# Kernel optimization log

Hardware: AMD Instinct MI355X
Metric: run time of the kernel (lower is better)

The kernel has to match this reference:

```python
import jax, jax.numpy as jnp
import numpy as np
from jax import lax

B, T, D, R, V = 128, 8, 2048, 4, 512

def setup_inputs() -> dict:
    key = jax.random.key(0)
    k0, k1, k2, k3, k4 = jax.random.split(key, 5)
    # scales chosen so the TT products stay within fp32 range (see notes)
    input_embs = jax.random.normal(k0, (B, T, D), dtype=jnp.float32) * 0.1
    label_ids = jax.random.randint(k1, (B, T), 0, V)
    w_alpha = jax.random.normal(k2, (D, R), dtype=jnp.float32) * 0.04
    w_beta = jax.random.normal(k3, (D, R), dtype=jnp.float32) * 0.04
    w_vocab = jax.random.normal(k4, (D, V * R * R), dtype=jnp.float32) * 0.04
    return {"input_embs": input_embs, "label_ids": label_ids,
            "w_alpha": w_alpha, "w_beta": w_beta, "w_vocab": w_vocab}

def _tt_loss(input_embs, w_alpha, w_beta, w_vocab, label_ids):
    b, t, d = input_embs.shape
    flat = input_embs.reshape(-1, d)                    # [B*T, D]
    alpha = jnp.abs((flat @ w_alpha).reshape(b, t, R).mean(1))   # [B, R]
    beta = jnp.abs((flat @ w_beta).reshape(b, t, R).mean(1))     # [B, R]
    core = jnp.abs((flat @ w_vocab).reshape(b, t, R, V, R).mean(1))  # [B, R, V, R]

    # --- _select: gather per-position R x R cores and chain-multiply ---
    core_v = core.transpose(0, 2, 1, 3)                 # [B, V, R, R]
    sel = jnp.take_along_axis(core_v, label_ids[:, :, None, None], axis=1)  # [B, T, R, R]
    sel_t = jnp.swapaxes(sel, 0, 1)                     # [T, B, R, R]

    def chain(carry, m):
        return jnp.einsum('bik,bkj->bij', carry, m), None
    res, _ = lax.scan(chain, sel_t[0], sel_t[1:])       # [B, R, R]
    u = jnp.einsum('bi,bij,bj->b', alpha, res, beta)    # unnormalized probs [B]

    # --- normalization constant: marg^(T+1) contracted with alpha/beta ---
    marg = core.sum(2)                                  # [B, R, R]

    def pow_step(c, _):
        return jnp.einsum('bik,bkj->bij', c, marg), None
    zmat, _ = lax.scan(pow_step, marg, None, length=t)  # marg^(t+1)
    z = jnp.einsum('bi,bij,bj->b', alpha, zmat, beta)

    loss = -jnp.log(u / z)
    return loss.mean()

def reference(input_embs, label_ids, w_alpha, w_beta, w_vocab):
    return _tt_loss(input_embs, w_alpha, w_beta, w_vocab, label_ids)
```

## Files before the change

kernel.cpp:

```cpp
#include <hip/hip_runtime.h>
#include <math.h>

#define BB 128
#define TT 8
#define DD 2048
#define RR 4
#define VV 512

typedef __attribute__((ext_vector_type(8))) short short8;
typedef __attribute__((ext_vector_type(4))) float v4f;

__device__ __forceinline__ unsigned pack_bf16(float x, float y) {
    union { float f; unsigned u; } a, b;
    a.f = x; b.f = y;
    unsigned ua = a.u + 0x7fffu + ((a.u >> 16) & 1u);
    unsigned ub = b.u + 0x7fffu + ((b.u >> 16) & 1u);
    return (ua >> 16) | (ub & 0xffff0000u);
}

__global__ __launch_bounds__(256) void phaseA(const float* __restrict__ inp,
                                              const float* __restrict__ w_alpha,
                                              const float* __restrict__ w_beta,
                                              unsigned short* __restrict__ fmb,
                                              float* __restrict__ alphaP,
                                              float* __restrict__ betaP,
                                              float* __restrict__ marg) {
    int bid = blockIdx.x;
    int b = bid >> 1, half = bid & 1;
    int tid = threadIdx.x;

    if (bid < 8) marg[bid * 256 + tid] = 0.f;

    const float* base = inp + (size_t)b * TT * DD;
    float pa[4] = {0.f, 0.f, 0.f, 0.f};
    float pb[4] = {0.f, 0.f, 0.f, 0.f};
#pragma unroll
    for (int i = 0; i < 4; ++i) {
        int d = half * 1024 + i * 256 + tid;
        float s = 0.f;
#pragma unroll
        for (int t = 0; t < TT; ++t) s += base[t * DD + d];
        float v = s * (1.0f / TT);
        union { float f; unsigned u; } cv; cv.f = v;
        unsigned r = cv.u + 0x7fffu + ((cv.u >> 16) & 1u);
        fmb[b * DD + d] = (unsigned short)(r >> 16);
        float4 wa = *(const float4*)(w_alpha + d * 4);
        float4 wb = *(const float4*)(w_beta + d * 4);
        pa[0] += v * wa.x; pa[1] += v * wa.y; pa[2] += v * wa.z; pa[3] += v * wa.w;
        pb[0] += v * wb.x; pb[1] += v * wb.y; pb[2] += v * wb.z; pb[3] += v * wb.w;
    }
#pragma unroll
    for (int r = 0; r < 4; ++r) {
        for (int m = 1; m < 64; m <<= 1) {
            pa[r] += __shfl_xor(pa[r], m);
            pb[r] += __shfl_xor(pb[r], m);
        }
    }
    __shared__ float sA[4][4], sB[4][4];
    int wid = tid >> 6;
    if ((tid & 63) == 0) {
#pragma unroll
        for (int r = 0; r < 4; ++r) { sA[wid][r] = pa[r]; sB[wid][r] = pb[r]; }
    }
    __syncthreads();
    if (tid < 4) {
        alphaP[b * 8 + half * 4 + tid] = sA[0][tid] + sA[1][tid] + sA[2][tid] + sA[3][tid];
        betaP [b * 8 + half * 4 + tid] = sB[0][tid] + sB[1][tid] + sB[2][tid] + sB[3][tid];
    }
}

__global__ __launch_bounds__(512, 2) void phaseB(const unsigned short* __restrict__ fmb,
                                                 const float* __restrict__ wv,
                                                 const int* __restrict__ labels,
                                                 float* __restrict__ margA,
                                                 float* __restrict__ sel) {
    __shared__ unsigned short Ws[2][32][136];
    __shared__ int slab[BB * TT];

    const int tid = threadIdx.x;
    const int nb = blockIdx.x;
    const int col0 = nb * 32;

    slab[tid] = labels[tid];
    slab[tid + 512] = labels[tid + 512];

    const int nq = tid & 7;
    const int kp = tid >> 3;
    const int w = tid >> 6;
    const int lane = tid & 63;
    const int m15 = lane & 15;
    const int q = lane >> 4;

    const float* wbase = wv + (size_t)(2 * kp) * 8192 + col0 + nq * 4;
    const unsigned short* abase = fmb + (w * 16 + m15) * DD + q * 8;

    v4f acc0 = {0.f, 0.f, 0.f, 0.f};
    v4f acc1 = {0.f, 0.f, 0.f, 0.f};
    short8 afrA[4], afrB[4];
    float4 swA0, swA1, swB0, swB1;

    swA0 = *(const float4*)(wbase);
    swA1 = *(const float4*)(wbase + 8192);
    {
        const float* p = wbase + (size_t)128 * 8192;
        swB0 = *(const float4*)(p);
        swB1 = *(const float4*)(p + 8192);
    }
#pragma unroll
    for (int ks = 0; ks < 4; ++ks) afrA[ks] = *(const short8*)(abase + ks * 32);
    {
        const float* f0 = (const float*)&swA0;
        const float* f1 = (const float*)&swA1;
#pragma unroll
        for (int j = 0; j < 4; ++j)
            *(unsigned*)&Ws[0][nq * 4 + j][2 * kp] = pack_bf16(f0[j], f1[j]);
    }
    __syncthreads();

    for (int i = 0; i < 8; ++i) {
        const int c0 = 2 * i;
        if (c0 < 14) {
            const float* p = wbase + (size_t)(c0 + 2) * 128 * 8192;
            swA0 = *(const float4*)(p);
            swA1 = *(const float4*)(p + 8192);
        }
        {
            const unsigned short* ap = abase + (c0 + 1) * 128;
#pragma unroll
            for (int ks = 0; ks < 4; ++ks) afrB[ks] = *(const short8*)(ap + ks * 32);
        }
#pragma unroll
        for (int ks = 0; ks < 4; ++ks) {
            short8 b0 = *(const short8*)&Ws[0][m15][ks * 32 + q * 8];
            short8 b1 = *(const short8*)&Ws[0][16 + m15][ks * 32 + q * 8];
            acc0 = __builtin_amdgcn_mfma_f32_16x16x32_bf16(afrA[ks], b0, acc0, 0, 0, 0);
            acc1 = __builtin_amdgcn_mfma_f32_16x16x32_bf16(afrA[ks], b1, acc1, 0, 0, 0);
        }
        {
            const float* f0 = (const float*)&swB0;
            const float* f1 = (const float*)&swB1;
#pragma unroll
            for (int j = 0; j < 4; ++j)
                *(unsigned*)&Ws[1][nq * 4 + j][2 * kp] = pack_bf16(f0[j], f1[j]);
        }
        __syncthreads();

        const int c1 = 2 * i + 1;
        if (c1 < 14) {
            const float* p = wbase + (size_t)(c1 + 2) * 128 * 8192;
            swB0 = *(const float4*)(p);
            swB1 = *(const float4*)(p + 8192);
        }
        if (c1 < 15) {
            const unsigned short* ap = abase + (c1 + 1) * 128;
#pragma unroll
            for (int ks = 0; ks < 4; ++ks) afrA[ks] = *(const short8*)(ap + ks * 32);
        }
#pragma unroll
        for (int ks = 0; ks < 4; ++ks) {
            short8 b0 = *(const short8*)&Ws[1][m15][ks * 32 + q * 8];
            short8 b1 = *(const short8*)&Ws[1][16 + m15][ks * 32 + q * 8];
            acc0 = __builtin_amdgcn_mfma_f32_16x16x32_bf16(afrB[ks], b0, acc0, 0, 0, 0);
            acc1 = __builtin_amdgcn_mfma_f32_16x16x32_bf16(afrB[ks], b1, acc1, 0, 0, 0);
        }
        if (c1 < 15) {
            const float* f0 = (const float*)&swA0;
            const float* f1 = (const float*)&swA1;
#pragma unroll
            for (int j = 0; j < 4; ++j)
                *(unsigned*)&Ws[0][nq * 4 + j][2 * kp] = pack_bf16(f0[j], f1[j]);
        }
        __syncthreads();
    }

    const int vbase = (nb & 63) * 8;
    const int iblk = nb >> 6;
    const int j = m15 & 3;
    const int v0 = vbase + (m15 >> 2);
    const float* a0p = (const float*)&acc0;
    const float* a1p = (const float*)&acc1;
#pragma unroll
    for (int r = 0; r < 4; ++r) {
        int m = w * 16 + q * 4 + r;
        float a0 = fabsf(a0p[r]);
        float a1 = fabsf(a1p[r]);
        float s = a0 + a1;
        s += __shfl_xor(s, 4);
        s += __shfl_xor(s, 8);
        if ((lane & 12) == 0) atomicAdd(&margA[m * 16 + iblk * 4 + j], s);
#pragma unroll
        for (int t = 0; t < TT; ++t) {
            int lv = slab[m * 8 + t];
            if (lv == v0)     sel[(m * 8 + t) * 16 + iblk * 4 + j] = a0;
            if (lv == v0 + 4) sel[(m * 8 + t) * 16 + iblk * 4 + j] = a1;
        }
    }
}

__global__ __launch_bounds__(128) void phaseD(const float* __restrict__ alphaP,
                                              const float* __restrict__ betaP,
                                              const float* __restrict__ marg,
                                              const float* __restrict__ sel,
                                              float* __restrict__ out) {
    int b = threadIdx.x;
    const float* sb = sel + b * TT * 16;
    float res[16], tmp[16], mm[16], zm[16];
#pragma unroll
    for (int e = 0; e < 16; ++e) res[e] = sb[e];
    for (int t = 1; t < TT; ++t) {
        const float* m = sb + t * 16;
#pragma unroll
        for (int i = 0; i < 4; ++i)
#pragma unroll
            for (int jj = 0; jj < 4; ++jj) {
                float s = 0.f;
#pragma unroll
                for (int k = 0; k < 4; ++k) s += res[i * 4 + k] * m[k * 4 + jj];
                tmp[i * 4 + jj] = s;
            }
#pragma unroll
        for (int e = 0; e < 16; ++e) res[e] = tmp[e];
    }
#pragma unroll
    for (int e = 0; e < 16; ++e) { mm[e] = marg[b * 16 + e]; zm[e] = mm[e]; }
    for (int st = 0; st < TT; ++st) {
#pragma unroll
        for (int i = 0; i < 4; ++i)
#pragma unroll
            for (int jj = 0; jj < 4; ++jj) {
                float s = 0.f;
#pragma unroll
                for (int k = 0; k < 4; ++k) s += zm[i * 4 + k] * mm[k * 4 + jj];
                tmp[i * 4 + jj] = s;
            }
#pragma unroll
        for (int e = 0; e < 16; ++e) zm[e] = tmp[e];
    }
    float u = 0.f, z = 0.f;
#pragma unroll
    for (int i = 0; i < 4; ++i) {
        float ai = fabsf(alphaP[b * 8 + i] + alphaP[b * 8 + 4 + i]);
#pragma unroll
        for (int jj = 0; jj < 4; ++jj) {
            float bj = fabsf(betaP[b * 8 + jj] + betaP[b * 8 + 4 + jj]);
            u += ai * res[i * 4 + jj] * bj;
            z += ai * zm[i * 4 + jj] * bj;
        }
    }
    float loss = logf(z) - logf(u);
    __shared__ float red[128];
    red[b] = loss;
    __syncthreads();
    for (int off = 64; off >= 1; off >>= 1) {
        if (b < off) red[b] += red[b + off];
        __syncthreads();
    }
    if (b == 0) out[0] = red[0] * (1.0f / BB);
}

extern "C" void kernel_launch(void* const* d_in, const int* in_sizes, int n_in,
                              void* d_out, int out_size, void* d_ws, size_t ws_size,
                              hipStream_t stream) {
    const float* inp     = (const float*)d_in[0];
    const int*   labels  = (const int*)d_in[1];
    const float* w_alpha = (const float*)d_in[2];
    const float* w_beta  = (const float*)d_in[3];
    const float* wv      = (const float*)d_in[4];
    float* out = (float*)d_out;

    float* ws     = (float*)d_ws;
    float* alphaP = ws;
    float* betaP  = ws + 1024;
    float* marg   = ws + 2048;
    float* sel    = ws + 4096;
    unsigned short* fmb = (unsigned short*)(ws + 20480);

    phaseA<<<256, 256, 0, stream>>>(inp, w_alpha, w_beta, fmb, alphaP, betaP, marg);
    phaseB<<<256, 512, 0, stream>>>(fmb, wv, labels, marg, sel);
    phaseD<<<1, 128, 0, stream>>>(alphaP, betaP, marg, sel, out);
}
```

Before: 122.6 us.

## Narrow phaseB column tiles to 16 and double K-chunk per stage with 512 blocks

The vocab GEMM kernel now handles 16 output columns per block instead of 32 and stages 256-row K chunks instead of 128. This doubles the grid to 512 blocks, and blocks are remapped so that neighbouring block IDs take columns spread across the weight matrix. The goal is more parallelism across CUs and fewer pipeline stages and barriers. In exchange, each block loads the full bf16 activation matrix, so activation traffic doubles, and register pressure rises from the 8-wide A fragments.

Measured after the change: 140.9 us. 14.9% more time.

```diff
diff --git a/kernel.cpp b/kernel.cpp
--- a/kernel.cpp
+++ b/kernel.cpp
@@ -69,23 +69,24 @@
     }
 }
 
-__global__ __launch_bounds__(512, 2) void phaseB(const unsigned short* __restrict__ fmb,
+__global__ __launch_bounds__(512, 4) void phaseB(const unsigned short* __restrict__ fmb,
                                                  const float* __restrict__ wv,
                                                  const int* __restrict__ labels,
                                                  float* __restrict__ margA,
                                                  float* __restrict__ sel) {
-    __shared__ unsigned short Ws[2][32][136];
+    __shared__ unsigned short Ws[2][16][268];
     __shared__ int slab[BB * TT];
 
     const int tid = threadIdx.x;
-    const int nb = blockIdx.x;
-    const int col0 = nb * 32;
+    const int bid = blockIdx.x;
+    const int nb = ((bid & 7) << 6) | (bid >> 3);
+    const int col0 = nb * 16;
 
     slab[tid] = labels[tid];
     slab[tid + 512] = labels[tid + 512];
 
-    const int nq = tid & 7;
-    const int kp = tid >> 3;
+    const int nq = tid & 3;
+    const int kp = tid >> 2;
     const int w = tid >> 6;
     const int lane = tid & 63;
     const int m15 = lane & 15;
@@ -94,20 +95,19 @@
     const float* wbase = wv + (size_t)(2 * kp) * 8192 + col0 + nq * 4;
     const unsigned short* abase = fmb + (w * 16 + m15) * DD + q * 8;
 
-    v4f acc0 = {0.f, 0.f, 0.f, 0.f};
-    v4f acc1 = {0.f, 0.f, 0.f, 0.f};
-    short8 afrA[4], afrB[4];
+    v4f acc = {0.f, 0.f, 0.f, 0.f};
+    short8 afrA[8], afrB[8];
     float4 swA0, swA1, swB0, swB1;
 
     swA0 = *(const float4*)(wbase);
     swA1 = *(const float4*)(wbase + 8192);
     {
-        const float* p = wbase + (size_t)128 * 8192;
+        const float* p = wbase + (size_t)256 * 8192;
         swB0 = *(const float4*)(p);
         swB1 = *(const float4*)(p + 8192);
     }
 #pragma unroll
-    for (int ks = 0; ks < 4; ++ks) afrA[ks] = *(const short8*)(abase + ks * 32);
+    for (int ks = 0; ks < 8; ++ks) afrA[ks] = *(const short8*)(abase + ks * 32);
     {
         const float* f0 = (const float*)&swA0;
         const float* f1 = (const float*)&swA1;
@@ -117,24 +117,23 @@
     }
     __syncthreads();
 
-    for (int i = 0; i < 8; ++i) {
+#pragma unroll
+    for (int i = 0; i < 4; ++i) {
         const int c0 = 2 * i;
-        if (c0 < 14) {
-            const float* p = wbase + (size_t)(c0 + 2) * 128 * 8192;
+        if (c0 < 6) {
+            const float* p = wbase + (size_t)(c0 + 2) * 256 * 8192;
             swA0 = *(const float4*)(p);
             swA1 = *(const float4*)(p + 8192);
         }
         {
-            const unsigned short* ap = abase + (c0 + 1) * 128;
-#pragma unroll
-            for (int ks = 0; ks < 4; ++ks) afrB[ks] = *(const short8*)(ap + ks * 32);
-        }
-#pragma unroll
-        for (int ks = 0; ks < 4; ++ks) {
+            const unsigned short* ap = abase + (c0 + 1) * 256;
+#pragma unroll
+            for (int ks = 0; ks < 8; ++ks) afrB[ks] = *(const short8*)(ap + ks * 32);
+        }
+#pragma unroll
+        for (int ks = 0; ks < 8; ++ks) {
             short8 b0 = *(const short8*)&Ws[0][m15][ks * 32 + q * 8];
-            short8 b1 = *(const short8*)&Ws[0][16 + m15][ks * 32 + q * 8];
-            acc0 = __builtin_amdgcn_mfma_f32_16x16x32_bf16(afrA[ks], b0, acc0, 0, 0, 0);
-            acc1 = __builtin_amdgcn_mfma_f32_16x16x32_bf16(afrA[ks], b1, acc1, 0, 0, 0);
+            acc = __builtin_amdgcn_mfma_f32_16x16x32_bf16(afrA[ks], b0, acc, 0, 0, 0);
         }
         {
             const float* f0 = (const float*)&swB0;
@@ -146,24 +145,22 @@
         __syncthreads();
 
         const int c1 = 2 * i + 1;
-        if (c1 < 14) {
-            const float* p = wbase + (size_t)(c1 + 2) * 128 * 8192;
+        if (c1 < 6) {
+            const float* p = wbase + (size_t)(c1 + 2) * 256 * 8192;
             swB0 = *(const float4*)(p);
             swB1 = *(const float4*)(p + 8192);
         }
-        if (c1 < 15) {
-            const unsigned short* ap = abase + (c1 + 1) * 128;
-#pragma unroll
-            for (int ks = 0; ks < 4; ++ks) afrA[ks] = *(const short8*)(ap + ks * 32);
-        }
-#pragma unroll
-        for (int ks = 0; ks < 4; ++ks) {
-            short8 b0 = *(const short8*)&Ws[1][m15][ks * 32 + q * 8];
-            short8 b1 = *(const short8*)&Ws[1][16 + m15][ks * 32 + q * 8];
-            acc0 = __builtin_amdgcn_mfma_f32_16x16x32_bf16(afrB[ks], b0, acc0, 0, 0, 0);
-            acc1 = __builtin_amdgcn_mfma_f32_16x16x32_bf16(afrB[ks], b1, acc1, 0, 0, 0);
-        }
-        if (c1 < 15) {
+        if (c1 < 7) {
+            const unsigned short* ap = abase + (c1 + 1) * 256;
+#pragma unroll
+            for (int ks = 0; ks < 8; ++ks) afrA[ks] = *(const short8*)(ap + ks * 32);
+        }
+#pragma unroll
+        for (int ks = 0; ks < 8; ++ks) {
+            short8 b1 = *(const short8*)&Ws[1][m15][ks * 32 + q * 8];
+            acc = __builtin_amdgcn_mfma_f32_16x16x32_bf16(afrB[ks], b1, acc, 0, 0, 0);
+        }
+        if (c1 < 7) {
             const float* f0 = (const float*)&swA0;
             const float* f1 = (const float*)&swA1;
 #pragma unroll
@@ -173,26 +170,22 @@
         __syncthreads();
     }
 
-    const int vbase = (nb & 63) * 8;
-    const int iblk = nb >> 6;
+    const int i_out = nb >> 7;
     const int j = m15 & 3;
-    const int v0 = vbase + (m15 >> 2);
-    const float* a0p = (const float*)&acc0;
-    const float* a1p = (const float*)&acc1;
+    const int v0 = (nb & 127) * 4 + (m15 >> 2);
+    const float* ap = (const float*)&acc;
 #pragma unroll
     for (int r = 0; r < 4; ++r) {
         int m = w * 16 + q * 4 + r;
-        float a0 = fabsf(a0p[r]);
-        float a1 = fabsf(a1p[r]);
-        float s = a0 + a1;
+        float a0 = fabsf(ap[r]);
+        float s = a0;
         s += __shfl_xor(s, 4);
         s += __shfl_xor(s, 8);
-        if ((lane & 12) == 0) atomicAdd(&margA[m * 16 + iblk * 4 + j], s);
+        if ((lane & 12) == 0) atomicAdd(&margA[m * 16 + i_out * 4 + j], s);
 #pragma unroll
         for (int t = 0; t < TT; ++t) {
             int lv = slab[m * 8 + t];
-            if (lv == v0)     sel[(m * 8 + t) * 16 + iblk * 4 + j] = a0;
-            if (lv == v0 + 4) sel[(m * 8 + t) * 16 + iblk * 4 + j] = a1;
+            if (lv == v0) sel[(m * 8 + t) * 16 + i_out * 4 + j] = a0;
         }
     }
 }
@@ -276,6 +269,6 @@
     unsigned short* fmb = (unsigned short*)(ws + 20480);
 
     phaseA<<<256, 256, 0, stream>>>(inp, w_alpha, w_beta, fmb, alphaP, betaP, marg);
-    phaseB<<<256, 512, 0, stream>>>(fmb, wv, labels, marg, sel);
+    phaseB<<<512, 512, 0, stream>>>(fmb, wv, labels, marg, sel);
     phaseD<<<1, 128, 0, stream>>>(alphaP, betaP, marg, sel, out);
 }
```

## Split GEMM K dimension across two blocks and add reduction kernel for marg/sel

Applied to the files above, without the earlier changes.

The main GEMM kernel now splits the 2048-long reduction dimension into two halves, launching 512 blocks instead of 256 and raising the launch-bounds occupancy hint. Raw partial results are written to a workspace buffer. A new kernel sums the two partials, applies abs, computes the vocab-marginal and gathers the label-selected cores, replacing the atomics and label scan in the GEMM epilogue. This is meant to fill more compute units and shorten each block's serial K loop, at the cost of writing and rereading an 8 MB partial buffer and one extra launch.

Result: no change. 122.5 us (-0.1%).

```diff
diff --git a/kernel.cpp b/kernel.cpp
--- a/kernel.cpp
+++ b/kernel.cpp
@@ -23,13 +23,10 @@
                                               const float* __restrict__ w_beta,
                                               unsigned short* __restrict__ fmb,
                                               float* __restrict__ alphaP,
-                                              float* __restrict__ betaP,
-                                              float* __restrict__ marg) {
+                                              float* __restrict__ betaP) {
     int bid = blockIdx.x;
     int b = bid >> 1, half = bid & 1;
     int tid = threadIdx.x;
-
-    if (bid < 8) marg[bid * 256 + tid] = 0.f;
 
     const float* base = inp + (size_t)b * TT * DD;
     float pa[4] = {0.f, 0.f, 0.f, 0.f};
@@ -69,20 +66,16 @@
     }
 }
 
-__global__ __launch_bounds__(512, 2) void phaseB(const unsigned short* __restrict__ fmb,
+__global__ __launch_bounds__(512, 4) void phaseB(const unsigned short* __restrict__ fmb,
                                                  const float* __restrict__ wv,
-                                                 const int* __restrict__ labels,
-                                                 float* __restrict__ margA,
-                                                 float* __restrict__ sel) {
+                                                 float* __restrict__ Cpart) {
     __shared__ unsigned short Ws[2][32][136];
-    __shared__ int slab[BB * TT];
 
     const int tid = threadIdx.x;
-    const int nb = blockIdx.x;
-    const int col0 = nb * 32;
-
-    slab[tid] = labels[tid];
-    slab[tid + 512] = labels[tid + 512];
+    const int bid = blockIdx.x;
+    const int colb = bid & 255;
+    const int half = bid >> 8;
+    const int col0 = colb * 32;
 
     const int nq = tid & 7;
     const int kp = tid >> 3;
@@ -91,8 +84,8 @@
     const int m15 = lane & 15;
     const int q = lane >> 4;
 
-    const float* wbase = wv + (size_t)(2 * kp) * 8192 + col0 + nq * 4;
-    const unsigned short* abase = fmb + (w * 16 + m15) * DD + q * 8;
+    const float* wbase = wv + (size_t)(half * 1024 + 2 * kp) * 8192 + col0 + nq * 4;
+    const unsigned short* abase = fmb + (w * 16 + m15) * DD + half * 1024 + q * 8;
 
     v4f acc0 = {0.f, 0.f, 0.f, 0.f};
     v4f acc1 = {0.f, 0.f, 0.f, 0.f};
@@ -117,9 +110,10 @@
     }
     __syncthreads();
 
-    for (int i = 0; i < 8; ++i) {
+#pragma unroll
+    for (int i = 0; i < 4; ++i) {
         const int c0 = 2 * i;
-        if (c0 < 14) {
+        if (c0 < 6) {
             const float* p = wbase + (size_t)(c0 + 2) * 128 * 8192;
             swA0 = *(const float4*)(p);
             swA1 = *(const float4*)(p + 8192);
@@ -146,12 +140,12 @@
         __syncthreads();
 
         const int c1 = 2 * i + 1;
-        if (c1 < 14) {
+        if (c1 < 6) {
             const float* p = wbase + (size_t)(c1 + 2) * 128 * 8192;
             swB0 = *(const float4*)(p);
             swB1 = *(const float4*)(p + 8192);
         }
-        if (c1 < 15) {
+        if (c1 < 7) {
             const unsigned short* ap = abase + (c1 + 1) * 128;
 #pragma unroll
             for (int ks = 0; ks < 4; ++ks) afrA[ks] = *(const short8*)(ap + ks * 32);
@@ -163,7 +157,7 @@
             acc0 = __builtin_amdgcn_mfma_f32_16x16x32_bf16(afrB[ks], b0, acc0, 0, 0, 0);
             acc1 = __builtin_amdgcn_mfma_f32_16x16x32_bf16(afrB[ks], b1, acc1, 0, 0, 0);
         }
-        if (c1 < 15) {
+        if (c1 < 7) {
             const float* f0 = (const float*)&swA0;
             const float* f1 = (const float*)&swA1;
 #pragma unroll
@@ -173,27 +167,54 @@
         __syncthreads();
     }
 
-    const int vbase = (nb & 63) * 8;
-    const int iblk = nb >> 6;
-    const int j = m15 & 3;
-    const int v0 = vbase + (m15 >> 2);
+    float* cbase = Cpart + (size_t)half * 128 * 8192 + col0 + m15;
     const float* a0p = (const float*)&acc0;
     const float* a1p = (const float*)&acc1;
 #pragma unroll
     for (int r = 0; r < 4; ++r) {
-        int m = w * 16 + q * 4 + r;
-        float a0 = fabsf(a0p[r]);
-        float a1 = fabsf(a1p[r]);
-        float s = a0 + a1;
-        s += __shfl_xor(s, 4);
-        s += __shfl_xor(s, 8);
-        if ((lane & 12) == 0) atomicAdd(&margA[m * 16 + iblk * 4 + j], s);
-#pragma unroll
-        for (int t = 0; t < TT; ++t) {
-            int lv = slab[m * 8 + t];
-            if (lv == v0)     sel[(m * 8 + t) * 16 + iblk * 4 + j] = a0;
-            if (lv == v0 + 4) sel[(m * 8 + t) * 16 + iblk * 4 + j] = a1;
-        }
+        int row = w * 16 + q * 4 + r;
+        cbase[(size_t)row * 8192]      = a0p[r];
+        cbase[(size_t)row * 8192 + 16] = a1p[r];
+    }
+}
+
+__global__ __launch_bounds__(256) void phaseC(const float* __restrict__ Cpart,
+                                              const int* __restrict__ labels,
+                                              float* __restrict__ marg,
+                                              float* __restrict__ sel) {
+    const int m = blockIdx.x;
+    const int tid = threadIdx.x;
+    const float* r0 = Cpart + (size_t)m * 8192;
+    const float* r1 = Cpart + (size_t)(128 + m) * 8192;
+
+    float pj[4] = {0.f, 0.f, 0.f, 0.f};
+    const int base = tid * 32;
+#pragma unroll
+    for (int g = 0; g < 8; ++g) {
+        float4 a = *(const float4*)(r0 + base + g * 4);
+        float4 b = *(const float4*)(r1 + base + g * 4);
+        pj[0] += fabsf(a.x + b.x);
+        pj[1] += fabsf(a.y + b.y);
+        pj[2] += fabsf(a.z + b.z);
+        pj[3] += fabsf(a.w + b.w);
+    }
+#pragma unroll
+    for (int j = 0; j < 4; ++j)
+        for (int s = 1; s < 64; s <<= 1) pj[j] += __shfl_xor(pj[j], s);
+    const int lane = tid & 63;
+    const int w = tid >> 6;
+    if (lane == 0) {
+#pragma unroll
+        for (int j = 0; j < 4; ++j) marg[m * 16 + w * 4 + j] = pj[j];
+    }
+
+    if (tid < 128) {
+        const int t = tid >> 4;
+        const int ij = tid & 15;
+        const int i = ij >> 2, j = ij & 3;
+        const int lv = labels[m * 8 + t];
+        const int col = i * 2048 + lv * 4 + j;
+        sel[(m * 8 + t) * 16 + ij] = fabsf(r0[col] + r1[col]);
     }
 }
 
@@ -274,8 +295,10 @@
     float* marg   = ws + 2048;
     float* sel    = ws + 4096;
     unsigned short* fmb = (unsigned short*)(ws + 20480);
-
-    phaseA<<<256, 256, 0, stream>>>(inp, w_alpha, w_beta, fmb, alphaP, betaP, marg);
-    phaseB<<<256, 512, 0, stream>>>(fmb, wv, labels, marg, sel);
+    float* Cpart  = ws + 151552;
+
+    phaseA<<<256, 256, 0, stream>>>(inp, w_alpha, w_beta, fmb, alphaP, betaP);
+    phaseB<<<512, 512, 0, stream>>>(fmb, wv, Cpart);
+    phaseC<<<128, 256, 0, stream>>>(Cpart, labels, marg, sel);
     phaseD<<<1, 128, 0, stream>>>(alphaP, betaP, marg, sel, out);
 }
```
